# Kernel tuning notes

Hardware: AMD Instinct MI355X
Metric: run time of the kernel (lower is better)

Reference implementation:

```python
import jax, jax.numpy as jnp
import numpy as np

GRID_SIZE = 8
IN_DIM = 1024
OUT_DIM = 1024
BATCH = 4096


def setup_inputs() -> dict:
    key = jax.random.key(0)
    k1, k2, k3 = jax.random.split(key, 3)
    noise_scale = 0.1
    noise_scale_base = 0.1
    x = jax.random.normal(k1, (BATCH, IN_DIM), dtype=jnp.float32)
    scale_base = (1.0 / np.sqrt(IN_DIM)
                  + (jax.random.normal(k2, (OUT_DIM, IN_DIM), dtype=jnp.float32) * 2 - 1)
                  * noise_scale_base)
    scale_spline = jnp.full((OUT_DIM, IN_DIM), 1.0, dtype=jnp.float32)
    coeff = (jax.random.uniform(k3, (2, OUT_DIM, IN_DIM, GRID_SIZE), dtype=jnp.float32)
             * noise_scale / (np.sqrt(IN_DIM) * np.sqrt(GRID_SIZE)))
    return {"x": x, "scale_base": scale_base, "scale_spline": scale_spline,
            "coeff": coeff}


def reference(x, scale_base, scale_spline, coeff):
    # x: (B, I); scale_base/scale_spline: (O, I); coeff: (2, O, I, G)
    G = coeff.shape[-1]
    k = jnp.arange(1, G + 1, dtype=x.dtype)          # (G,)
    ang = x[:, :, None] * k                           # (B, I, G)
    cos_b = jnp.cos(ang)
    sin_b = jnp.sin(ang)
    # fold scale_spline into coeff: (2, O, I, G)
    w = scale_spline[None, :, :, None] * coeff
    spline = (jnp.einsum('big,oig->bo', cos_b, w[0])
              + jnp.einsum('big,oig->bo', sin_b, w[1]))  # (B, O)
    base = jnp.einsum('bi,oi->bo', jax.nn.silu(x), scale_base)
    return base + spline
```

## Files before the change

### kernel.cpp

```cpp
#include <hip/hip_runtime.h>
#include <hip/hip_bf16.h>
#include <stdint.h>

#define BATCH   4096
#define IN_DIM  1024
#define OUT_DIM 1024
#define GRID_G  8
#define K8      16384
#define KB      1024
#define SPLIT8  4
#define WSCALE  256.0f

typedef __bf16 bf16x8 __attribute__((ext_vector_type(8)));
typedef float  f32x4  __attribute__((ext_vector_type(4)));
typedef int    i32x4  __attribute__((ext_vector_type(4)));
typedef int    i32x8  __attribute__((ext_vector_type(8)));

__device__ inline void store_fp8x8(void* p, const float v[8]) {
    int lo = 0, hi = 0;
    lo = __builtin_amdgcn_cvt_pk_fp8_f32(v[0], v[1], lo, false);
    lo = __builtin_amdgcn_cvt_pk_fp8_f32(v[2], v[3], lo, true);
    hi = __builtin_amdgcn_cvt_pk_fp8_f32(v[4], v[5], hi, false);
    hi = __builtin_amdgcn_cvt_pk_fp8_f32(v[6], v[7], hi, true);
    *(int2*)p = make_int2(lo, hi);
}

__global__ void prep(const float* __restrict__ x, const float* __restrict__ sb,
                     const float* __restrict__ ss, const float* __restrict__ coeff,
                     uint8_t* __restrict__ A8, uint8_t* __restrict__ W8,
                     __bf16* __restrict__ Ab, __bf16* __restrict__ Wb) {
    if (blockIdx.x < 2048) {
        int t  = blockIdx.x * blockDim.x + threadIdx.x;
        int b  = t >> 7;
        int i0 = (t & 127) * 8;
        const float4* xp = (const float4*)(x + (size_t)b * IN_DIM + i0);
        float4 x0 = xp[0], x1 = xp[1];
        float xv[8] = {x0.x, x0.y, x0.z, x0.w, x1.x, x1.y, x1.z, x1.w};

        float c1[8], s1[8], ck[8], sk[8];
        bf16x8 v;
#pragma unroll
        for (int j = 0; j < 8; ++j) {
            float sil = xv[j] / (1.f + __expf(-xv[j]));
            v[j] = (__bf16)sil;
            __sincosf(xv[j], &s1[j], &c1[j]);
            ck[j] = c1[j]; sk[j] = s1[j];
        }
        *(bf16x8*)(Ab + (size_t)b * IN_DIM + i0) = v;

        uint8_t* a8 = A8 + (size_t)b * K8 + i0;
#pragma unroll
        for (int g = 1; g <= GRID_G; ++g) {
            float vc[8], vs[8];
#pragma unroll
            for (int j = 0; j < 8; ++j) {
                vc[j] = ck[j];
                vs[j] = sk[j];
                float cn = ck[j] * c1[j] - sk[j] * s1[j];
                float sn = sk[j] * c1[j] + ck[j] * s1[j];
                ck[j] = cn; sk[j] = sn;
            }
            store_fp8x8(a8 + (size_t)(g - 1) * IN_DIM, vc);
            store_fp8x8(a8 + (size_t)(GRID_G + g - 1) * IN_DIM, vs);
        }
    } else {
        int t  = (blockIdx.x - 2048) * blockDim.x + threadIdx.x;
        int o  = t >> 7;
        int i0 = (t & 127) * 8;
        size_t oi = (size_t)o * IN_DIM + i0;

        float s[8];
        {
            const float4* sp = (const float4*)(ss + oi);
            float4 s0 = sp[0], s1 = sp[1];
            s[0]=s0.x; s[1]=s0.y; s[2]=s0.z; s[3]=s0.w;
            s[4]=s1.x; s[5]=s1.y; s[6]=s1.z; s[7]=s1.w;
        }
        {
            const float4* bp = (const float4*)(sb + oi);
            float4 b0 = bp[0], b1 = bp[1];
            float bv[8] = {b0.x, b0.y, b0.z, b0.w, b1.x, b1.y, b1.z, b1.w};
            bf16x8 v;
#pragma unroll
            for (int j = 0; j < 8; ++j) v[j] = (__bf16)bv[j];
            *(bf16x8*)(Wb + oi) = v;
        }
        uint8_t* w8 = W8 + (size_t)o * K8 + i0;
#pragma unroll
        for (int p = 0; p < 2; ++p) {
            const float* cp = coeff + ((size_t)p * OUT_DIM * IN_DIM + oi) * GRID_G;
            float c[8][8];
#pragma unroll
            for (int j = 0; j < 8; ++j) {
                const float4* cj = (const float4*)(cp + (size_t)j * GRID_G);
                float4 a0 = cj[0], a1 = cj[1];
                c[j][0]=a0.x; c[j][1]=a0.y; c[j][2]=a0.z; c[j][3]=a0.w;
                c[j][4]=a1.x; c[j][5]=a1.y; c[j][6]=a1.z; c[j][7]=a1.w;
            }
#pragma unroll
            for (int g = 0; g < GRID_G; ++g) {
                float v[8];
#pragma unroll
                for (int j = 0; j < 8; ++j) v[j] = s[j] * c[j][g] * WSCALE;
                store_fp8x8(w8 + (size_t)(p * GRID_G + g) * IN_DIM, v);
            }
        }
    }
}

__global__ __launch_bounds__(256, 4) void gemm_all(const uint8_t* __restrict__ A8,
                                                   const uint8_t* __restrict__ W8,
                                                   const uint8_t* __restrict__ Ab,
                                                   const uint8_t* __restrict__ Wb,
                                                   float* __restrict__ C) {
    __shared__ __align__(16) uint8_t As[16384];
    __shared__ __align__(16) uint8_t Bs[16384];
    const int tid = threadIdx.x;
    const int w   = tid >> 6;
    const int l   = tid & 63;
    const int bn  = blockIdx.x;
    const int bm  = blockIdx.y;
    const int kz  = blockIdx.z;
    const int wm  = w & 1;
    const int wn  = w >> 1;

    f32x4 acc[4][4] = {};

    const int srow   = l >> 3;
    const int schunk = ((l & 7) ^ srow) * 16;
    const int lm = l & 15;
    const int q  = l >> 4;
    float oscale;

    if (kz < SPLIT8) {
        const uint8_t* Ag = A8 + (size_t)(bm * 128 + w * 32 + srow) * K8 + kz * (K8 / SPLIT8) + schunk;
        const uint8_t* Bg = W8 + (size_t)(bn * 128 + w * 32 + srow) * K8 + kz * (K8 / SPLIT8) + schunk;
        const int c0 = (q * 2) << 4, c1 = (q * 2 + 1) << 4;

        for (int ks = 0; ks < (K8 / SPLIT8) / 128; ++ks) {
#pragma unroll
            for (int j = 0; j < 4; ++j) {
                __builtin_amdgcn_global_load_lds(
                    (const uint32_t*)(Ag + (size_t)(j * 8) * K8),
                    (uint32_t*)(As + (w * 32 + j * 8) * 128), 16, 0, 0);
                __builtin_amdgcn_global_load_lds(
                    (const uint32_t*)(Bg + (size_t)(j * 8) * K8),
                    (uint32_t*)(Bs + (w * 32 + j * 8) * 128), 16, 0, 0);
            }
            Ag += 128; Bg += 128;
            __syncthreads();

            i32x8 bf[4];
#pragma unroll
            for (int j = 0; j < 4; ++j) {
                const int row = wn * 64 + j * 16 + lm;
                const int sw  = (row & 7) << 4;
                const uint8_t* rp = Bs + row * 128;
                i32x4 lo = *(const i32x4*)(rp + (c0 ^ sw));
                i32x4 hi = *(const i32x4*)(rp + (c1 ^ sw));
                bf[j] = __builtin_shufflevector(lo, hi, 0, 1, 2, 3, 4, 5, 6, 7);
            }
#pragma unroll
            for (int i = 0; i < 4; ++i) {
                const int row = wm * 64 + i * 16 + lm;
                const int sw  = (row & 7) << 4;
                const uint8_t* rp = As + row * 128;
                i32x4 lo = *(const i32x4*)(rp + (c0 ^ sw));
                i32x4 hi = *(const i32x4*)(rp + (c1 ^ sw));
                i32x8 af = __builtin_shufflevector(lo, hi, 0, 1, 2, 3, 4, 5, 6, 7);
#pragma unroll
                for (int j = 0; j < 4; ++j)
                    acc[i][j] = __builtin_amdgcn_mfma_scale_f32_16x16x128_f8f6f4(
                        af, bf[j], acc[i][j], 0, 0, 0, 0x7f7f7f7f, 0, 0x7f7f7f7f);
            }
            __syncthreads();
        }
        oscale = 1.0f / WSCALE;
    } else {
        const uint8_t* Ag = Ab + (size_t)(bm * 128 + w * 32 + srow) * (KB * 2) + schunk;
        const uint8_t* Bg = Wb + (size_t)(bn * 128 + w * 32 + srow) * (KB * 2) + schunk;

        for (int ks = 0; ks < (KB * 2) / 128; ++ks) {
#pragma unroll
            for (int j = 0; j < 4; ++j) {
                __builtin_amdgcn_global_load_lds(
                    (const uint32_t*)(Ag + (size_t)(j * 8) * (KB * 2)),
                    (uint32_t*)(As + (w * 32 + j * 8) * 128), 16, 0, 0);
                __builtin_amdgcn_global_load_lds(
                    (const uint32_t*)(Bg + (size_t)(j * 8) * (KB * 2)),
                    (uint32_t*)(Bs + (w * 32 + j * 8) * 128), 16, 0, 0);
            }
            Ag += 128; Bg += 128;
            __syncthreads();

#pragma unroll
            for (int h = 0; h < 2; ++h) {
                bf16x8 af[4], bfr[4];
#pragma unroll
                for (int i = 0; i < 4; ++i) {
                    const int row = wm * 64 + i * 16 + lm;
                    af[i] = *(const bf16x8*)(As + row * 128 + ((((h * 4 + q) ^ (row & 7))) << 4));
                }
#pragma unroll
                for (int j = 0; j < 4; ++j) {
                    const int row = wn * 64 + j * 16 + lm;
                    bfr[j] = *(const bf16x8*)(Bs + row * 128 + ((((h * 4 + q) ^ (row & 7))) << 4));
                }
#pragma unroll
                for (int i = 0; i < 4; ++i)
#pragma unroll
                    for (int j = 0; j < 4; ++j)
                        acc[i][j] = __builtin_amdgcn_mfma_f32_16x16x32_bf16(af[i], bfr[j], acc[i][j], 0, 0, 0);
            }
            __syncthreads();
        }
        oscale = 1.0f;
    }

    const int row0 = bm * 128 + wm * 64 + q * 4;
    const int col0 = bn * 128 + wn * 64 + lm;
#pragma unroll
    for (int i = 0; i < 4; ++i)
#pragma unroll
        for (int j = 0; j < 4; ++j)
#pragma unroll
            for (int r = 0; r < 4; ++r)
                unsafeAtomicAdd(&C[(size_t)(row0 + i * 16 + r) * OUT_DIM + col0 + j * 16],
                                acc[i][j][r] * oscale);
}

extern "C" void kernel_launch(void* const* d_in, const int* in_sizes, int n_in,
                              void* d_out, int out_size, void* d_ws, size_t ws_size,
                              hipStream_t stream) {
    const float* x     = (const float*)d_in[0];
    const float* sb    = (const float*)d_in[1];
    const float* ss    = (const float*)d_in[2];
    const float* coeff = (const float*)d_in[3];
    float* out = (float*)d_out;

    uint8_t* A8 = (uint8_t*)d_ws;
    uint8_t* W8 = A8 + (size_t)BATCH * K8;
    __bf16*  Ab = (__bf16*)(W8 + (size_t)OUT_DIM * K8);
    __bf16*  Wb = Ab + (size_t)BATCH * KB;

    hipLaunchKernelGGL(prep, dim3(2048 + 512), dim3(256), 0, stream,
                       x, sb, ss, coeff, A8, W8, Ab, Wb);
    hipMemsetAsync(out, 0, (size_t)BATCH * OUT_DIM * sizeof(float), stream);
    hipLaunchKernelGGL(gemm_all, dim3(OUT_DIM / 128, BATCH / 128, SPLIT8 + 1), dim3(256), 0, stream,
                       A8, W8, (const uint8_t*)Ab, (const uint8_t*)Wb, out);
}
```

Baseline: 276.8 us.

## Split prep into feature/weight kernels, fuse output zeroing, remap GEMM tiles per XCD

The single prep kernel becomes two. The feature kernel handles 16 elements per thread with wider 16-byte fp8 stores, and it also zeroes the output buffer, so the separate memset is gone. The weight kernel uses 4 elements per thread, which gives more threads and better-coalesced coefficient reads. The GEMM block indices are remapped so that blocks landing on the same XCD share neighbouring A/B tiles for L2 reuse. The risks are one extra kernel launch and higher register pressure in the feature kernel.

```diff
diff --git a/kernel.cpp b/kernel.cpp
--- a/kernel.cpp
+++ b/kernel.cpp
@@ -12,98 +12,114 @@
 #define WSCALE  256.0f
 
 typedef __bf16 bf16x8 __attribute__((ext_vector_type(8)));
+typedef __bf16 bf16x4 __attribute__((ext_vector_type(4)));
 typedef float  f32x4  __attribute__((ext_vector_type(4)));
 typedef int    i32x4  __attribute__((ext_vector_type(4)));
 typedef int    i32x8  __attribute__((ext_vector_type(8)));
 
-__device__ inline void store_fp8x8(void* p, const float v[8]) {
-    int lo = 0, hi = 0;
-    lo = __builtin_amdgcn_cvt_pk_fp8_f32(v[0], v[1], lo, false);
-    lo = __builtin_amdgcn_cvt_pk_fp8_f32(v[2], v[3], lo, true);
-    hi = __builtin_amdgcn_cvt_pk_fp8_f32(v[4], v[5], hi, false);
-    hi = __builtin_amdgcn_cvt_pk_fp8_f32(v[6], v[7], hi, true);
-    *(int2*)p = make_int2(lo, hi);
-}
-
-__global__ void prep(const float* __restrict__ x, const float* __restrict__ sb,
-                     const float* __restrict__ ss, const float* __restrict__ coeff,
-                     uint8_t* __restrict__ A8, uint8_t* __restrict__ W8,
-                     __bf16* __restrict__ Ab, __bf16* __restrict__ Wb) {
-    if (blockIdx.x < 2048) {
-        int t  = blockIdx.x * blockDim.x + threadIdx.x;
-        int b  = t >> 7;
-        int i0 = (t & 127) * 8;
+__global__ __launch_bounds__(256) void prep_feat(const float* __restrict__ x,
+                                                 uint8_t* __restrict__ A8,
+                                                 __bf16* __restrict__ Ab,
+                                                 float* __restrict__ C) {
+    const int t  = blockIdx.x * 256 + threadIdx.x;
+    const int b  = t >> 6;
+    const int i0 = (t & 63) * 16;
+
+    {
+        float4 z = make_float4(0.f, 0.f, 0.f, 0.f);
+        float4* cz = (float4*)(C + (size_t)t * 16);
+        cz[0] = z; cz[1] = z; cz[2] = z; cz[3] = z;
+    }
+
+    float xv[16];
+    {
         const float4* xp = (const float4*)(x + (size_t)b * IN_DIM + i0);
-        float4 x0 = xp[0], x1 = xp[1];
-        float xv[8] = {x0.x, x0.y, x0.z, x0.w, x1.x, x1.y, x1.z, x1.w};
-
-        float c1[8], s1[8], ck[8], sk[8];
-        bf16x8 v;
-#pragma unroll
-        for (int j = 0; j < 8; ++j) {
-            float sil = xv[j] / (1.f + __expf(-xv[j]));
-            v[j] = (__bf16)sil;
-            __sincosf(xv[j], &s1[j], &c1[j]);
-            ck[j] = c1[j]; sk[j] = s1[j];
-        }
-        *(bf16x8*)(Ab + (size_t)b * IN_DIM + i0) = v;
-
-        uint8_t* a8 = A8 + (size_t)b * K8 + i0;
-#pragma unroll
-        for (int g = 1; g <= GRID_G; ++g) {
-            float vc[8], vs[8];
-#pragma unroll
-            for (int j = 0; j < 8; ++j) {
-                vc[j] = ck[j];
-                vs[j] = sk[j];
+        float4 q0 = xp[0], q1 = xp[1], q2 = xp[2], q3 = xp[3];
+        xv[0]=q0.x;  xv[1]=q0.y;  xv[2]=q0.z;  xv[3]=q0.w;
+        xv[4]=q1.x;  xv[5]=q1.y;  xv[6]=q1.z;  xv[7]=q1.w;
+        xv[8]=q2.x;  xv[9]=q2.y;  xv[10]=q2.z; xv[11]=q2.w;
+        xv[12]=q3.x; xv[13]=q3.y; xv[14]=q3.z; xv[15]=q3.w;
+    }
+
+    float c1[16], s1[16], ck[16], sk[16];
+    bf16x8 va, vb;
+#pragma unroll
+    for (int j = 0; j < 16; ++j) {
+        float e  = __expf(-xv[j]);
+        float sl = xv[j] * __builtin_amdgcn_rcpf(1.f + e);
+        if (j < 8) va[j & 7] = (__bf16)sl; else vb[j & 7] = (__bf16)sl;
+        s1[j] = __sinf(xv[j]);
+        c1[j] = __cosf(xv[j]);
+        ck[j] = c1[j]; sk[j] = s1[j];
+    }
+    *(bf16x8*)(Ab + (size_t)b * IN_DIM + i0)     = va;
+    *(bf16x8*)(Ab + (size_t)b * IN_DIM + i0 + 8) = vb;
+
+    uint8_t* a8 = A8 + (size_t)b * K8 + i0;
+#pragma unroll
+    for (int g = 0; g < GRID_G; ++g) {
+        i32x4 wc, ws;
+#pragma unroll
+        for (int q = 0; q < 4; ++q) {
+            int dc = 0, ds = 0;
+            dc = __builtin_amdgcn_cvt_pk_fp8_f32(ck[4*q+0], ck[4*q+1], dc, false);
+            dc = __builtin_amdgcn_cvt_pk_fp8_f32(ck[4*q+2], ck[4*q+3], dc, true);
+            ds = __builtin_amdgcn_cvt_pk_fp8_f32(sk[4*q+0], sk[4*q+1], ds, false);
+            ds = __builtin_amdgcn_cvt_pk_fp8_f32(sk[4*q+2], sk[4*q+3], ds, true);
+            wc[q] = dc; ws[q] = ds;
+        }
+        *(i32x4*)(a8 + (size_t)g * IN_DIM)            = wc;
+        *(i32x4*)(a8 + (size_t)(GRID_G + g) * IN_DIM) = ws;
+        if (g < GRID_G - 1) {
+#pragma unroll
+            for (int j = 0; j < 16; ++j) {
                 float cn = ck[j] * c1[j] - sk[j] * s1[j];
                 float sn = sk[j] * c1[j] + ck[j] * s1[j];
                 ck[j] = cn; sk[j] = sn;
             }
-            store_fp8x8(a8 + (size_t)(g - 1) * IN_DIM, vc);
-            store_fp8x8(a8 + (size_t)(GRID_G + g - 1) * IN_DIM, vs);
-        }
-    } else {
-        int t  = (blockIdx.x - 2048) * blockDim.x + threadIdx.x;
-        int o  = t >> 7;
-        int i0 = (t & 127) * 8;
-        size_t oi = (size_t)o * IN_DIM + i0;
-
-        float s[8];
-        {
-            const float4* sp = (const float4*)(ss + oi);
-            float4 s0 = sp[0], s1 = sp[1];
-            s[0]=s0.x; s[1]=s0.y; s[2]=s0.z; s[3]=s0.w;
-            s[4]=s1.x; s[5]=s1.y; s[6]=s1.z; s[7]=s1.w;
-        }
-        {
-            const float4* bp = (const float4*)(sb + oi);
-            float4 b0 = bp[0], b1 = bp[1];
-            float bv[8] = {b0.x, b0.y, b0.z, b0.w, b1.x, b1.y, b1.z, b1.w};
-            bf16x8 v;
-#pragma unroll
-            for (int j = 0; j < 8; ++j) v[j] = (__bf16)bv[j];
-            *(bf16x8*)(Wb + oi) = v;
-        }
-        uint8_t* w8 = W8 + (size_t)o * K8 + i0;
-#pragma unroll
-        for (int p = 0; p < 2; ++p) {
-            const float* cp = coeff + ((size_t)p * OUT_DIM * IN_DIM + oi) * GRID_G;
-            float c[8][8];
-#pragma unroll
-            for (int j = 0; j < 8; ++j) {
-                const float4* cj = (const float4*)(cp + (size_t)j * GRID_G);
-                float4 a0 = cj[0], a1 = cj[1];
-                c[j][0]=a0.x; c[j][1]=a0.y; c[j][2]=a0.z; c[j][3]=a0.w;
-                c[j][4]=a1.x; c[j][5]=a1.y; c[j][6]=a1.z; c[j][7]=a1.w;
-            }
-#pragma unroll
-            for (int g = 0; g < GRID_G; ++g) {
-                float v[8];
-#pragma unroll
-                for (int j = 0; j < 8; ++j) v[j] = s[j] * c[j][g] * WSCALE;
-                store_fp8x8(w8 + (size_t)(p * GRID_G + g) * IN_DIM, v);
-            }
+        }
+    }
+}
+
+__global__ __launch_bounds__(256) void prep_w(const float* __restrict__ sb,
+                                              const float* __restrict__ ss,
+                                              const float* __restrict__ coeff,
+                                              uint8_t* __restrict__ W8,
+                                              __bf16* __restrict__ Wb) {
+    const int t  = blockIdx.x * 256 + threadIdx.x;
+    const int o  = t >> 8;
+    const int i0 = (t & 255) * 4;
+    const size_t oi = (size_t)o * IN_DIM + i0;
+
+    const float4 s4 = *(const float4*)(ss + oi);
+    const float  s[4] = {s4.x * WSCALE, s4.y * WSCALE, s4.z * WSCALE, s4.w * WSCALE};
+
+    {
+        float4 b4 = *(const float4*)(sb + oi);
+        bf16x4 w;
+        w[0] = (__bf16)b4.x; w[1] = (__bf16)b4.y;
+        w[2] = (__bf16)b4.z; w[3] = (__bf16)b4.w;
+        *(bf16x4*)(Wb + oi) = w;
+    }
+
+    uint8_t* w8 = W8 + (size_t)o * K8 + i0;
+#pragma unroll
+    for (int p = 0; p < 2; ++p) {
+        const float* cp = coeff + ((size_t)p * OUT_DIM * IN_DIM + oi) * GRID_G;
+        float c[4][8];
+#pragma unroll
+        for (int j = 0; j < 4; ++j) {
+            const float4* cj = (const float4*)(cp + (size_t)j * GRID_G);
+            float4 a0 = cj[0], a1 = cj[1];
+            c[j][0]=a0.x; c[j][1]=a0.y; c[j][2]=a0.z; c[j][3]=a0.w;
+            c[j][4]=a1.x; c[j][5]=a1.y; c[j][6]=a1.z; c[j][7]=a1.w;
+        }
+#pragma unroll
+        for (int g = 0; g < GRID_G; ++g) {
+            int d = 0;
+            d = __builtin_amdgcn_cvt_pk_fp8_f32(s[0]*c[0][g], s[1]*c[1][g], d, false);
+            d = __builtin_amdgcn_cvt_pk_fp8_f32(s[2]*c[2][g], s[3]*c[3][g], d, true);
+            *(int*)(w8 + (size_t)(p * GRID_G + g) * IN_DIM) = d;
         }
     }
 }
@@ -118,8 +134,11 @@
     const int tid = threadIdx.x;
     const int w   = tid >> 6;
     const int l   = tid & 63;
-    const int bn  = blockIdx.x;
-    const int bm  = blockIdx.y;
+    const int flat = blockIdx.y * 8 + blockIdx.x;
+    const int xcd  = flat & 7;
+    const int idx  = flat >> 3;
+    const int bn   = (xcd & 1) * 4 + (idx & 3);
+    const int bm   = (xcd >> 1) * 8 + (idx >> 2);
     const int kz  = blockIdx.z;
     const int wm  = w & 1;
     const int wn  = w >> 1;
@@ -243,9 +262,10 @@
     __bf16*  Ab = (__bf16*)(W8 + (size_t)OUT_DIM * K8);
     __bf16*  Wb = Ab + (size_t)BATCH * KB;
 
-    hipLaunchKernelGGL(prep, dim3(2048 + 512), dim3(256), 0, stream,
-                       x, sb, ss, coeff, A8, W8, Ab, Wb);
-    hipMemsetAsync(out, 0, (size_t)BATCH * OUT_DIM * sizeof(float), stream);
+    hipLaunchKernelGGL(prep_feat, dim3(BATCH * IN_DIM / 16 / 256), dim3(256), 0, stream,
+                       x, A8, Ab, out);
+    hipLaunchKernelGGL(prep_w, dim3(OUT_DIM * IN_DIM / 4 / 256), dim3(256), 0, stream,
+                       sb, ss, coeff, W8, Wb);
     hipLaunchKernelGGL(gemm_all, dim3(OUT_DIM / 128, BATCH / 128, SPLIT8 + 1), dim3(256), 0, stream,
                        A8, W8, (const uint8_t*)Ab, (const uint8_t*)Wb, out);
 }
```

After: 255.1 us. 7.8% less time.
